# Performance work log

Measured on AMD Instinct MI355X. Metric: run time of the kernel, lower is better.

Reference implementation:

```python
import jax, jax.numpy as jnp
import numpy as np

N = 50000      # nodes
E = 800000     # edges (avg degree 16)
IN, H, OUT = 128, 128, 64
NEG_SLOPE = 0.01  # F.leaky_relu default


def _glorot(key, shape):
    lim = float(np.sqrt(6.0 / (shape[0] + shape[1])))
    return jax.random.uniform(key, shape, jnp.float32, -lim, lim)


def setup_inputs() -> dict:
    key = jax.random.key(0)
    ks = jax.random.split(key, 12)
    x = jax.random.normal(ks[0], (N, IN), jnp.float32)
    edge_index = jax.random.randint(ks[1], (2, E), 0, N, dtype=jnp.int64)
    edge_weight = jax.random.uniform(ks[2], (E,), jnp.float32)
    params = {}
    dims = [(IN, H), (H, H), (H, H), (H, OUT)]
    for i, (di, do) in enumerate(dims, start=1):
        params[f"W{i}"] = _glorot(ks[2 + i], (di, do))
        params[f"b{i}"] = jnp.zeros((do,), jnp.float32)
    return {"x": x, "edge_index": edge_index, "edge_weight": edge_weight, **params}


def _gcn_norm(edge_index, edge_weight, n):
    # PyG gcn_norm: add self-loops with weight 1, symmetric D^-1/2 A D^-1/2
    loop = jnp.arange(n, dtype=edge_index.dtype)
    row = jnp.concatenate([edge_index[0], loop])   # source
    col = jnp.concatenate([edge_index[1], loop])   # target
    w = jnp.concatenate([edge_weight, jnp.ones((n,), edge_weight.dtype)])
    deg = jax.ops.segment_sum(w, col, num_segments=n)
    dinv = jnp.where(deg > 0, jax.lax.rsqrt(deg), 0.0)
    norm = dinv[row] * w * dinv[col]
    return row, col, norm


def _gcn_conv(x, W, b, row, col, norm, n):
    h = x @ W                                   # [N, out] dense GEMM
    msg = h[row] * norm[:, None]                # gather + edge scale  [E+N, out]
    out = jax.ops.segment_sum(msg, col, num_segments=n)  # scatter-add
    return out + b


def reference(x, edge_index, edge_weight, W1, b1, W2, b2, W3, b3, W4, b4):
    n = x.shape[0]
    row, col, norm = _gcn_norm(edge_index, edge_weight, n)  # identical for all layers
    h = _gcn_conv(x, W1, b1, row, col, norm, n)
    h = jax.nn.leaky_relu(h, NEG_SLOPE)
    # dropout (p=0.25) is identity in eval mode
    h = _gcn_conv(h, W2, b2, row, col, norm, n)
    h = jax.nn.leaky_relu(h, NEG_SLOPE)
    h = _gcn_conv(h, W3, b3, row, col, norm, n)
    h = jax.nn.leaky_relu(h, NEG_SLOPE)
    h = _gcn_conv(h, W4, b4, row, col, norm, n)
    return h
```

## Files before the change

### kernel.cpp

```cpp
#include <hip/hip_runtime.h>
#include <hip/hip_bf16.h>


#define CAP 64


__global__ void fillcap_k(const int* __restrict__ ei, const float* __restrict__ ew,
                          int* __restrict__ fillc, int2* __restrict__ ed, int E) {
    int e = blockIdx.x * 256 + threadIdx.x;
    if (e >= E) return;
    int r = ei[e];
    int c = ei[E + e];
    int pos = atomicAdd(&fillc[c], 1);
    if (pos < CAP) {
        ed[(size_t)c * CAP + pos] = make_int2(r, __float_as_int(ew[e]));
    }
}

__global__ void segdeg_k(const int* __restrict__ fillc, const int2* __restrict__ ed,
                         float* __restrict__ dinv, int n) {
    int t = blockIdx.x * 256 + threadIdx.x;
    int node = t >> 4, l = t & 15;
    if (node >= n) return;
    int len = min(fillc[node], CAP);
    float s = 0.f;
    for (int i = l; i < len; i += 16) s += __int_as_float(ed[(size_t)node * CAP + i].y);
    #pragma unroll
    for (int d = 1; d < 16; d <<= 1) s += __shfl_xor(s, d);
    if (l == 0) dinv[node] = rsqrtf(s + 1.0f);
}

__global__ void nrmfix_k(const int* __restrict__ fillc, int2* __restrict__ ed,
                         const float* __restrict__ dinv, int n) {
    int t = blockIdx.x * 256 + threadIdx.x;
    int node = t >> 4, l = t & 15;
    if (node >= n) return;
    int len = min(fillc[node], CAP);
    float dc = dinv[node];
    for (int i = l; i < len; i += 16) {
        size_t idx = (size_t)node * CAP + i;
        int2 d = ed[idx];
        ((float*)&ed[idx])[1] = dinv[d.x] * __int_as_float(d.y) * dc;
    }
}


template <bool LEAKY>
__global__ __launch_bounds__(256) void aggcap128_k(
        const float* __restrict__ h, const int* __restrict__ fillc,
        const int2* __restrict__ ed, const float* __restrict__ dinv,
        const float* __restrict__ bias, float* __restrict__ out, int n) {
    int node = blockIdx.x * 4 + (threadIdx.x >> 6);
    if (node >= n) return;
    int lane = threadIdx.x & 63;
    int half = lane >> 5;
    int q = lane & 31;
    size_t beg = (size_t)node * CAP;
    int len = min(fillc[node], CAP);
    float4 acc = make_float4(0.f, 0.f, 0.f, 0.f);
    int e = 0;
    for (; e + 8 <= len; e += 8) {
        int2 d0 = ed[beg + e + 0 + half];
        int2 d1 = ed[beg + e + 2 + half];
        int2 d2 = ed[beg + e + 4 + half];
        int2 d3 = ed[beg + e + 6 + half];
        float4 v0 = *(const float4*)&h[(size_t)d0.x * 128 + q * 4];
        float4 v1 = *(const float4*)&h[(size_t)d1.x * 128 + q * 4];
        float4 v2 = *(const float4*)&h[(size_t)d2.x * 128 + q * 4];
        float4 v3 = *(const float4*)&h[(size_t)d3.x * 128 + q * 4];
        float w0 = __int_as_float(d0.y), w1 = __int_as_float(d1.y);
        float w2 = __int_as_float(d2.y), w3 = __int_as_float(d3.y);
        acc.x += w0*v0.x; acc.y += w0*v0.y; acc.z += w0*v0.z; acc.w += w0*v0.w;
        acc.x += w1*v1.x; acc.y += w1*v1.y; acc.z += w1*v1.z; acc.w += w1*v1.w;
        acc.x += w2*v2.x; acc.y += w2*v2.y; acc.z += w2*v2.z; acc.w += w2*v2.w;
        acc.x += w3*v3.x; acc.y += w3*v3.y; acc.z += w3*v3.z; acc.w += w3*v3.w;
    }
    if (e < len) {
        #pragma unroll
        for (int t = 0; t < 4; ++t) {
            int j = e + 2 * t + half;
            bool ok = j < len;
            int2 d = ed[beg + (ok ? j : 0)];
            float w = ok ? __int_as_float(d.y) : 0.f;
            int sr = ok ? d.x : node;
            float4 v = *(const float4*)&h[(size_t)sr * 128 + q * 4];
            acc.x += w*v.x; acc.y += w*v.y; acc.z += w*v.z; acc.w += w*v.w;
        }
    }
    acc.x += __shfl_xor(acc.x, 32);
    acc.y += __shfl_xor(acc.y, 32);
    acc.z += __shfl_xor(acc.z, 32);
    acc.w += __shfl_xor(acc.w, 32);
    float di = dinv[node];
    float ws = di * di;
    float4 hv = *(const float4*)&h[(size_t)node * 128 + q * 4];
    float4 bb = *(const float4*)&bias[q * 4];
    acc.x += ws*hv.x + bb.x;
    acc.y += ws*hv.y + bb.y;
    acc.z += ws*hv.z + bb.z;
    acc.w += ws*hv.w + bb.w;
    if (LEAKY) {
        acc.x = acc.x > 0.f ? acc.x : 0.01f * acc.x;
        acc.y = acc.y > 0.f ? acc.y : 0.01f * acc.y;
        acc.z = acc.z > 0.f ? acc.z : 0.01f * acc.z;
        acc.w = acc.w > 0.f ? acc.w : 0.01f * acc.w;
    }
    if (half == 0) *(float4*)&out[(size_t)node * 128 + q * 4] = acc;
}

__global__ __launch_bounds__(256) void aggcap64_k(
        const float* __restrict__ h, const int* __restrict__ fillc,
        const int2* __restrict__ ed, const float* __restrict__ dinv,
        const float* __restrict__ bias, float* __restrict__ out, int n) {
    int node = blockIdx.x * 4 + (threadIdx.x >> 6);
    if (node >= n) return;
    int lane = threadIdx.x & 63;
    int qtr = lane >> 4;
    int q = lane & 15;
    size_t beg = (size_t)node * CAP;
    int len = min(fillc[node], CAP);
    float4 acc = make_float4(0.f, 0.f, 0.f, 0.f);
    int e = 0;
    for (; e + 8 <= len; e += 8) {
        int2 d0 = ed[beg + e + 0 + qtr];
        int2 d1 = ed[beg + e + 4 + qtr];
        float4 v0 = *(const float4*)&h[(size_t)d0.x * 64 + q * 4];
        float4 v1 = *(const float4*)&h[(size_t)d1.x * 64 + q * 4];
        float w0 = __int_as_float(d0.y), w1 = __int_as_float(d1.y);
        acc.x += w0*v0.x; acc.y += w0*v0.y; acc.z += w0*v0.z; acc.w += w0*v0.w;
        acc.x += w1*v1.x; acc.y += w1*v1.y; acc.z += w1*v1.z; acc.w += w1*v1.w;
    }
    if (e < len) {
        #pragma unroll
        for (int t = 0; t < 2; ++t) {
            int j = e + 4 * t + qtr;
            bool ok = j < len;
            int2 d = ed[beg + (ok ? j : 0)];
            float w = ok ? __int_as_float(d.y) : 0.f;
            int sr = ok ? d.x : node;
            float4 v = *(const float4*)&h[(size_t)sr * 64 + q * 4];
            acc.x += w*v.x; acc.y += w*v.y; acc.z += w*v.z; acc.w += w*v.w;
        }
    }
    acc.x += __shfl_xor(acc.x, 16);
    acc.y += __shfl_xor(acc.y, 16);
    acc.z += __shfl_xor(acc.z, 16);
    acc.w += __shfl_xor(acc.w, 16);
    acc.x += __shfl_xor(acc.x, 32);
    acc.y += __shfl_xor(acc.y, 32);
    acc.z += __shfl_xor(acc.z, 32);
    acc.w += __shfl_xor(acc.w, 32);
    float di = dinv[node];
    float ws = di * di;
    float4 hv = *(const float4*)&h[(size_t)node * 64 + q * 4];
    float4 bb = *(const float4*)&bias[q * 4];
    acc.x += ws*hv.x + bb.x;
    acc.y += ws*hv.y + bb.y;
    acc.z += ws*hv.z + bb.z;
    acc.w += ws*hv.w + bb.w;
    if (qtr == 0) *(float4*)&out[(size_t)node * 64 + q * 4] = acc;
}


template <int OUTD>
__global__ __launch_bounds__(512) void gemm_k(const float* __restrict__ A,
                                              const float* __restrict__ W,
                                              float* __restrict__ C, int nrows) {
    constexpr int CW = OUTD / 16;
    constexpr int WF4 = (32 * OUTD / 4) / 512;
    __shared__ float As[32][132];
    __shared__ float Ws[32][OUTD];
    const int t = threadIdx.x;
    const int rowbase = blockIdx.x * 128;
    const int tx = t & 15, ty = t >> 4;
    const int r0 = ty * 4, c0 = tx * CW;

    float acc[4][CW];
    #pragma unroll
    for (int i = 0; i < 4; ++i)
        #pragma unroll
        for (int j = 0; j < CW; ++j) acc[i][j] = 0.f;

    const int arow0 = t >> 3, akq0 = t & 7;
    const int arow1 = (t + 512) >> 3, akq1 = t & 7;

    auto loadA = [&](int kt, int row, int kq) -> float4 {
        int gr = rowbase + row;
        if (gr < nrows) return *(const float4*)&A[(size_t)gr * 128 + kt * 32 + kq * 4];
        return make_float4(0.f, 0.f, 0.f, 0.f);
    };
    auto stA = [&](int row, int kq, float4 v) {
        As[kq * 4 + 0][row] = v.x;
        As[kq * 4 + 1][row] = v.y;
        As[kq * 4 + 2][row] = v.z;
        As[kq * 4 + 3][row] = v.w;
    };

    stA(arow0, akq0, loadA(0, arow0, akq0));
    stA(arow1, akq1, loadA(0, arow1, akq1));
    #pragma unroll
    for (int u = 0; u < WF4; ++u) {
        int idx = t + u * 512;
        int k = idx / (OUTD / 4), cq = idx % (OUTD / 4);
        *(float4*)&Ws[k][cq * 4] = *(const float4*)&W[(size_t)k * OUTD + cq * 4];
    }
    __syncthreads();

    float4 pa0, pa1, pw[WF4];
    #pragma unroll
    for (int kt = 0; kt < 4; ++kt) {
        if (kt < 3) {
            pa0 = loadA(kt + 1, arow0, akq0);
            pa1 = loadA(kt + 1, arow1, akq1);
            #pragma unroll
            for (int u = 0; u < WF4; ++u) {
                int idx = t + u * 512;
                int k = idx / (OUTD / 4), cq = idx % (OUTD / 4);
                pw[u] = *(const float4*)&W[(size_t)((kt + 1) * 32 + k) * OUTD + cq * 4];
            }
        }
        #pragma unroll 8
        for (int k = 0; k < 32; ++k) {
            float4 a = *(const float4*)&As[k][r0];
            float w[CW];
            #pragma unroll
            for (int j = 0; j < CW; j += 4)
                *(float4*)&w[j] = *(const float4*)&Ws[k][c0 + j];
            #pragma unroll
            for (int j = 0; j < CW; ++j) {
                acc[0][j] += a.x * w[j];
                acc[1][j] += a.y * w[j];
                acc[2][j] += a.z * w[j];
                acc[3][j] += a.w * w[j];
            }
        }
        __syncthreads();
        if (kt < 3) {
            stA(arow0, akq0, pa0);
            stA(arow1, akq1, pa1);
            #pragma unroll
            for (int u = 0; u < WF4; ++u) {
                int idx = t + u * 512;
                int k = idx / (OUTD / 4), cq = idx % (OUTD / 4);
                *(float4*)&Ws[k][cq * 4] = pw[u];
            }
            __syncthreads();
        }
    }

    #pragma unroll
    for (int i = 0; i < 4; ++i) {
        int gr = rowbase + r0 + i;
        if (gr < nrows) {
            #pragma unroll
            for (int j = 0; j < CW; j += 4)
                *(float4*)&C[(size_t)gr * OUTD + c0 + j] = *(float4*)&acc[i][j];
        }
    }
}


__global__ void deg_cnt_k(const int* __restrict__ ei, const float* __restrict__ ew,
                          float* __restrict__ deg, int* __restrict__ cnt, int E) {
    int e = blockIdx.x * 256 + threadIdx.x;
    if (e >= E) return;
    int c = ei[E + e];
    atomicAdd(&deg[c], ew[e]);
    atomicAdd(&cnt[c], 1);
}

__global__ void dinv_k(float* __restrict__ d, int n) {
    int i = blockIdx.x * 256 + threadIdx.x;
    if (i >= n) return;
    d[i] = rsqrtf(d[i] + 1.0f);
}

__global__ void scan_blocks_k(const int* __restrict__ cnt, int* __restrict__ rowptr,
                              int* __restrict__ partials, int n) {
    int gid = blockIdx.x * 1024 + threadIdx.x;
    int v = (gid < n) ? cnt[gid] : 0;
    int lane = threadIdx.x & 63, wid = threadIdx.x >> 6;
    int x = v;
    #pragma unroll
    for (int d = 1; d < 64; d <<= 1) {
        int y = __shfl_up(x, d);
        if (lane >= d) x += y;
    }
    __shared__ int wsum[16];
    if (lane == 63) wsum[wid] = x;
    __syncthreads();
    if (wid == 0 && lane < 16) {
        int s = wsum[lane];
        #pragma unroll
        for (int d = 1; d < 16; d <<= 1) {
            int y = __shfl_up(s, d);
            if (lane >= d) s += y;
        }
        wsum[lane] = s;
    }
    __syncthreads();
    int inc = x + (wid > 0 ? wsum[wid - 1] : 0);
    if (gid < n) rowptr[gid] = inc - v;
    if (threadIdx.x == 1023) partials[blockIdx.x] = inc;
}

__global__ void scan_part_k(int* __restrict__ p, int nb) {
    int lane = threadIdx.x;
    int v = (lane < nb) ? p[lane] : 0;
    int x = v;
    #pragma unroll
    for (int d = 1; d < 64; d <<= 1) {
        int y = __shfl_up(x, d);
        if (lane >= d) x += y;
    }
    if (lane < nb) p[lane] = x - v;
    if (lane == 63) p[nb] = x;
}

__global__ void scan_add_k(int* __restrict__ rowptr, const int* __restrict__ p,
                           int n, int nb) {
    int i = blockIdx.x * 1024 + threadIdx.x;
    if (i < n) rowptr[i] += p[blockIdx.x];
    if (i == 0) rowptr[n] = p[nb];
}

__global__ void fill_k(const int* __restrict__ ei, const float* __restrict__ ew,
                       const float* __restrict__ dinv, const int* __restrict__ rowptr,
                       int* __restrict__ fillc, int* __restrict__ src,
                       float* __restrict__ nrm, int E) {
    int e = blockIdx.x * 256 + threadIdx.x;
    if (e >= E) return;
    int r = ei[e];
    int c = ei[E + e];
    int pos = rowptr[c] + atomicAdd(&fillc[c], 1);
    src[pos] = r;
    nrm[pos] = dinv[r] * ew[e] * dinv[c];
}

template <bool LEAKY>
__global__ __launch_bounds__(256) void agg128_k(
        const float* __restrict__ h, const int* __restrict__ rowptr,
        const int* __restrict__ src, const float* __restrict__ nrm,
        const float* __restrict__ dinv, const float* __restrict__ bias,
        float* __restrict__ out, int n) {
    int node = blockIdx.x * 4 + (threadIdx.x >> 6);
    if (node >= n) return;
    int lane = threadIdx.x & 63;
    int beg = rowptr[node], end = rowptr[node + 1];
    float2 acc = make_float2(0.f, 0.f);
    int e = beg;
    for (; e + 4 <= end; e += 4) {
        int s0 = src[e], s1 = src[e + 1], s2 = src[e + 2], s3 = src[e + 3];
        float w0 = nrm[e], w1 = nrm[e + 1], w2 = nrm[e + 2], w3 = nrm[e + 3];
        float2 v0 = *(const float2*)&h[(size_t)s0 * 128 + lane * 2];
        float2 v1 = *(const float2*)&h[(size_t)s1 * 128 + lane * 2];
        float2 v2 = *(const float2*)&h[(size_t)s2 * 128 + lane * 2];
        float2 v3 = *(const float2*)&h[(size_t)s3 * 128 + lane * 2];
        acc.x += w0 * v0.x; acc.y += w0 * v0.y;
        acc.x += w1 * v1.x; acc.y += w1 * v1.y;
        acc.x += w2 * v2.x; acc.y += w2 * v2.y;
        acc.x += w3 * v3.x; acc.y += w3 * v3.y;
    }
    for (; e < end; ++e) {
        int s = src[e];
        float w = nrm[e];
        float2 hv = *(const float2*)&h[(size_t)s * 128 + lane * 2];
        acc.x += w * hv.x;
        acc.y += w * hv.y;
    }
    float di = dinv[node];
    float ws = di * di;
    float2 hv = *(const float2*)&h[(size_t)node * 128 + lane * 2];
    acc.x += ws * hv.x;
    acc.y += ws * hv.y;
    float2 bb = *(const float2*)&bias[lane * 2];
    acc.x += bb.x;
    acc.y += bb.y;
    if (LEAKY) {
        acc.x = acc.x > 0.f ? acc.x : 0.01f * acc.x;
        acc.y = acc.y > 0.f ? acc.y : 0.01f * acc.y;
    }
    *(float2*)&out[(size_t)node * 128 + lane * 2] = acc;
}

__global__ __launch_bounds__(256) void agg64_k(
        const float* __restrict__ h, const int* __restrict__ rowptr,
        const int* __restrict__ src, const float* __restrict__ nrm,
        const float* __restrict__ dinv, const float* __restrict__ bias,
        float* __restrict__ out, int n) {
    int node = blockIdx.x * 4 + (threadIdx.x >> 6);
    if (node >= n) return;
    int lane = threadIdx.x & 63;
    int beg = rowptr[node], end = rowptr[node + 1];
    float acc = 0.f;
    int e = beg;
    for (; e + 4 <= end; e += 4) {
        int s0 = src[e], s1 = src[e + 1], s2 = src[e + 2], s3 = src[e + 3];
        float w0 = nrm[e], w1 = nrm[e + 1], w2 = nrm[e + 2], w3 = nrm[e + 3];
        acc += w0 * h[(size_t)s0 * 64 + lane];
        acc += w1 * h[(size_t)s1 * 64 + lane];
        acc += w2 * h[(size_t)s2 * 64 + lane];
        acc += w3 * h[(size_t)s3 * 64 + lane];
    }
    for (; e < end; ++e) {
        acc += nrm[e] * h[(size_t)src[e] * 64 + lane];
    }
    float di = dinv[node];
    acc += di * di * h[(size_t)node * 64 + lane];
    acc += bias[lane];
    out[(size_t)node * 64 + lane] = acc;
}


extern "C" void kernel_launch(void* const* d_in, const int* in_sizes, int n_in,
                              void* d_out, int out_size, void* d_ws, size_t ws_size,
                              hipStream_t stream) {
    const float* x  = (const float*)d_in[0];
    const int* ei   = (const int*)d_in[1];
    const float* ew = (const float*)d_in[2];
    const float* W1 = (const float*)d_in[3];
    const float* b1 = (const float*)d_in[4];
    const float* W2 = (const float*)d_in[5];
    const float* b2 = (const float*)d_in[6];
    const float* W3 = (const float*)d_in[7];
    const float* b3 = (const float*)d_in[8];
    const float* W4 = (const float*)d_in[9];
    const float* b4 = (const float*)d_in[10];

    const int N = in_sizes[0] / 128;
    const int E = in_sizes[1] / 2;

    auto alignup = [](size_t o) { return (o + 255) & ~(size_t)255; };
    char* ws = (char*)d_ws;
    (void)n_in; (void)out_size;

    int eb = (E + 255) / 256;
    int gb = (N + 127) / 128;
    int ab = (N + 3) / 4;
    int qb = (N * 16 + 255) / 256;

    size_t off = 0;
    float* dinv  = (float*)(ws + off); off = alignup(off + (size_t)N * 4);
    int*   fillc = (int*)(ws + off);   off = alignup(off + (size_t)N * 4);
    size_t zb_cap = off;
    int2*  ed    = (int2*)(ws + off);  off = alignup(off + (size_t)N * CAP * 8);
    float* hbufC = (float*)(ws + off); off = alignup(off + (size_t)N * 128 * 4);
    float* featC = (float*)(ws + off); off = alignup(off + (size_t)N * 128 * 4);
    size_t need_cap = off;

    if (need_cap <= ws_size) {
        hipMemsetAsync(d_ws, 0, zb_cap, stream);
        fillcap_k<<<eb, 256, 0, stream>>>(ei, ew, fillc, ed, E);
        segdeg_k<<<qb, 256, 0, stream>>>(fillc, ed, dinv, N);
        nrmfix_k<<<qb, 256, 0, stream>>>(fillc, ed, dinv, N);

        gemm_k<128><<<gb, 512, 0, stream>>>(x, W1, hbufC, N);
        aggcap128_k<true><<<ab, 256, 0, stream>>>(hbufC, fillc, ed, dinv, b1, featC, N);
        gemm_k<128><<<gb, 512, 0, stream>>>(featC, W2, hbufC, N);
        aggcap128_k<true><<<ab, 256, 0, stream>>>(hbufC, fillc, ed, dinv, b2, featC, N);
        gemm_k<128><<<gb, 512, 0, stream>>>(featC, W3, hbufC, N);
        aggcap128_k<true><<<ab, 256, 0, stream>>>(hbufC, fillc, ed, dinv, b3, featC, N);
        gemm_k<64><<<gb, 512, 0, stream>>>(featC, W4, hbufC, N);
        aggcap64_k<<<ab, 256, 0, stream>>>(hbufC, fillc, ed, dinv, b4, (float*)d_out, N);
        return;
    }

    off = 0;
    float* deg   = (float*)(ws + off); off = alignup(off + (size_t)N * 4);
    int*   cnt   = (int*)(ws + off);   off = alignup(off + (size_t)N * 4);
    int*   fillc2= (int*)(ws + off);   off = alignup(off + (size_t)N * 4);
    size_t zbytes = off;
    int*   rowptr = (int*)(ws + off);  off = alignup(off + (size_t)(N + 1) * 4);
    int*   parts  = (int*)(ws + off);  off = alignup(off + 64 * 4);
    int*   srcA   = (int*)(ws + off);  off = alignup(off + (size_t)E * 4);
    float* nrm    = (float*)(ws + off); off = alignup(off + (size_t)E * 4);
    float* hbuf   = (float*)(ws + off); off = alignup(off + (size_t)N * 128 * 4);
    float* feat   = (float*)(ws + off); off = alignup(off + (size_t)N * 128 * 4);

    hipMemsetAsync(d_ws, 0, zbytes, stream);

    int nb = (N + 255) / 256;
    int sb = (N + 1023) / 1024;

    deg_cnt_k<<<eb, 256, 0, stream>>>(ei, ew, deg, cnt, E);
    dinv_k<<<nb, 256, 0, stream>>>(deg, N);
    scan_blocks_k<<<sb, 1024, 0, stream>>>(cnt, rowptr, parts, N);
    scan_part_k<<<1, 64, 0, stream>>>(parts, sb);
    scan_add_k<<<sb, 1024, 0, stream>>>(rowptr, parts, N, sb);
    fill_k<<<eb, 256, 0, stream>>>(ei, ew, deg, rowptr, fillc2, srcA, nrm, E);

    gemm_k<128><<<gb, 512, 0, stream>>>(x, W1, hbuf, N);
    agg128_k<true><<<ab, 256, 0, stream>>>(hbuf, rowptr, srcA, nrm, deg, b1, feat, N);
    gemm_k<128><<<gb, 512, 0, stream>>>(feat, W2, hbuf, N);
    agg128_k<true><<<ab, 256, 0, stream>>>(hbuf, rowptr, srcA, nrm, deg, b2, feat, N);
    gemm_k<128><<<gb, 512, 0, stream>>>(feat, W3, hbuf, N);
    agg128_k<true><<<ab, 256, 0, stream>>>(hbuf, rowptr, srcA, nrm, deg, b3, feat, N);
    gemm_k<64><<<gb, 512, 0, stream>>>(feat, W4, hbuf, N);
    agg64_k<<<ab, 256, 0, stream>>>(hbuf, rowptr, srcA, nrm, deg, b4, (float*)d_out, N);
}
```

Before: 377.9 us.

## Fuse first GEMM with edge bucketing, enlarge GEMM thread tiles, unroll aggregation

Merges the first-layer GEMM and the capped edge-bucket fill into one launch, with blocks split by blockIdx, so that independent work can overlap and one launch is removed. The GEMM moves from 512 to 256 threads per block, each thread now computing 8 rows instead of 4, with launch bounds targeting 3 blocks per CU. This gives more register reuse per shared-memory load at the cost of higher register pressure. The aggregation kernels gain a 16-edge unrolled loop that issues more independent gathers per iteration to hide memory latency.

```diff
diff --git a/kernel.cpp b/kernel.cpp
--- a/kernel.cpp
+++ b/kernel.cpp
@@ -4,6 +4,128 @@
 
 #define CAP 64
 
+
+template <int OUTD>
+__device__ __forceinline__ void gemm_body(const float* __restrict__ A,
+                                          const float* __restrict__ W,
+                                          float* __restrict__ C, int nrows, int bid) {
+    constexpr int CW = OUTD / 16;
+    constexpr int WF4 = (32 * OUTD / 4) / 256;
+    __shared__ float As[32][132];
+    __shared__ float Ws[32][OUTD];
+    const int t = threadIdx.x;
+    const int rowbase = bid * 128;
+    const int tx = t & 15, ty = t >> 4;
+    const int r0 = ty * 8, c0 = tx * CW;
+
+    float acc[8][CW];
+    #pragma unroll
+    for (int i = 0; i < 8; ++i)
+        #pragma unroll
+        for (int j = 0; j < CW; ++j) acc[i][j] = 0.f;
+
+    const int arow = t >> 3, akq = t & 7;
+
+    auto loadA = [&](int kt, int row) -> float4 {
+        int gr = rowbase + row;
+        if (gr < nrows) return *(const float4*)&A[(size_t)gr * 128 + kt * 32 + akq * 4];
+        return make_float4(0.f, 0.f, 0.f, 0.f);
+    };
+    auto stA = [&](int row, float4 v) {
+        As[akq * 4 + 0][row] = v.x;
+        As[akq * 4 + 1][row] = v.y;
+        As[akq * 4 + 2][row] = v.z;
+        As[akq * 4 + 3][row] = v.w;
+    };
+
+    #pragma unroll
+    for (int u = 0; u < 4; ++u) stA(arow + u * 32, loadA(0, arow + u * 32));
+    #pragma unroll
+    for (int u = 0; u < WF4; ++u) {
+        int idx = t + u * 256;
+        int k = idx / (OUTD / 4), cq = idx % (OUTD / 4);
+        *(float4*)&Ws[k][cq * 4] = *(const float4*)&W[(size_t)k * OUTD + cq * 4];
+    }
+    __syncthreads();
+
+    float4 pa[4], pw[WF4];
+    #pragma unroll
+    for (int kt = 0; kt < 4; ++kt) {
+        if (kt < 3) {
+            #pragma unroll
+            for (int u = 0; u < 4; ++u) pa[u] = loadA(kt + 1, arow + u * 32);
+            #pragma unroll
+            for (int u = 0; u < WF4; ++u) {
+                int idx = t + u * 256;
+                int k = idx / (OUTD / 4), cq = idx % (OUTD / 4);
+                pw[u] = *(const float4*)&W[(size_t)((kt + 1) * 32 + k) * OUTD + cq * 4];
+            }
+        }
+        #pragma unroll 8
+        for (int k = 0; k < 32; ++k) {
+            float4 a0 = *(const float4*)&As[k][r0];
+            float4 a1 = *(const float4*)&As[k][r0 + 4];
+            float w[CW];
+            #pragma unroll
+            for (int j = 0; j < CW; j += 4)
+                *(float4*)&w[j] = *(const float4*)&Ws[k][c0 + j];
+            float ar[8] = {a0.x, a0.y, a0.z, a0.w, a1.x, a1.y, a1.z, a1.w};
+            #pragma unroll
+            for (int i = 0; i < 8; ++i)
+                #pragma unroll
+                for (int j = 0; j < CW; ++j)
+                    acc[i][j] += ar[i] * w[j];
+        }
+        __syncthreads();
+        if (kt < 3) {
+            #pragma unroll
+            for (int u = 0; u < 4; ++u) stA(arow + u * 32, pa[u]);
+            #pragma unroll
+            for (int u = 0; u < WF4; ++u) {
+                int idx = t + u * 256;
+                int k = idx / (OUTD / 4), cq = idx % (OUTD / 4);
+                *(float4*)&Ws[k][cq * 4] = pw[u];
+            }
+            __syncthreads();
+        }
+    }
+
+    #pragma unroll
+    for (int i = 0; i < 8; ++i) {
+        int gr = rowbase + r0 + i;
+        if (gr < nrows) {
+            #pragma unroll
+            for (int j = 0; j < CW; j += 4)
+                *(float4*)&C[(size_t)gr * OUTD + c0 + j] = *(float4*)&acc[i][j];
+        }
+    }
+}
+
+template <int OUTD>
+__global__ __launch_bounds__(256, 3) void gemm_k(const float* __restrict__ A,
+                                                 const float* __restrict__ W,
+                                                 float* __restrict__ C, int nrows) {
+    gemm_body<OUTD>(A, W, C, nrows, blockIdx.x);
+}
+
+__global__ __launch_bounds__(256, 3) void gemm1_fill_k(
+        const float* __restrict__ A, const float* __restrict__ W,
+        float* __restrict__ C, int nrows, int gb,
+        const int* __restrict__ ei, const float* __restrict__ ew,
+        int* __restrict__ fillc, int2* __restrict__ ed, int E) {
+    if ((int)blockIdx.x < gb) {
+        gemm_body<128>(A, W, C, nrows, blockIdx.x);
+        return;
+    }
+    int e = (blockIdx.x - gb) * 256 + threadIdx.x;
+    if (e >= E) return;
+    int r = ei[e];
+    int c = ei[E + e];
+    int pos = atomicAdd(&fillc[c], 1);
+    if (pos < CAP) {
+        ed[(size_t)c * CAP + pos] = make_int2(r, __float_as_int(ew[e]));
+    }
+}
 
 __global__ void fillcap_k(const int* __restrict__ ei, const float* __restrict__ ew,
                           int* __restrict__ fillc, int2* __restrict__ ed, int E) {
@@ -59,6 +181,21 @@
     int len = min(fillc[node], CAP);
     float4 acc = make_float4(0.f, 0.f, 0.f, 0.f);
     int e = 0;
+    for (; e + 16 <= len; e += 16) {
+        int2 d[8];
+        #pragma unroll
+        for (int u = 0; u < 8; ++u) d[u] = ed[beg + e + 2 * u + half];
+        float4 v[8];
+        #pragma unroll
+        for (int u = 0; u < 8; ++u)
+            v[u] = *(const float4*)&h[(size_t)d[u].x * 128 + q * 4];
+        #pragma unroll
+        for (int u = 0; u < 8; ++u) {
+            float w = __int_as_float(d[u].y);
+            acc.x += w * v[u].x; acc.y += w * v[u].y;
+            acc.z += w * v[u].z; acc.w += w * v[u].w;
+        }
+    }
     for (; e + 8 <= len; e += 8) {
         int2 d0 = ed[beg + e + 0 + half];
         int2 d1 = ed[beg + e + 2 + half];
@@ -121,6 +258,21 @@
     int len = min(fillc[node], CAP);
     float4 acc = make_float4(0.f, 0.f, 0.f, 0.f);
     int e = 0;
+    for (; e + 16 <= len; e += 16) {
+        int2 d[4];
+        #pragma unroll
+        for (int u = 0; u < 4; ++u) d[u] = ed[beg + e + 4 * u + qtr];
+        float4 v[4];
+        #pragma unroll
+        for (int u = 0; u < 4; ++u)
+            v[u] = *(const float4*)&h[(size_t)d[u].x * 64 + q * 4];
+        #pragma unroll
+        for (int u = 0; u < 4; ++u) {
+            float w = __int_as_float(d[u].y);
+            acc.x += w * v[u].x; acc.y += w * v[u].y;
+            acc.z += w * v[u].z; acc.w += w * v[u].w;
+        }
+    }
     for (; e + 8 <= len; e += 8) {
         int2 d0 = ed[beg + e + 0 + qtr];
         int2 d1 = ed[beg + e + 4 + qtr];
@@ -159,104 +311,6 @@
     acc.z += ws*hv.z + bb.z;
     acc.w += ws*hv.w + bb.w;
     if (qtr == 0) *(float4*)&out[(size_t)node * 64 + q * 4] = acc;
-}
-
-
-template <int OUTD>
-__global__ __launch_bounds__(512) void gemm_k(const float* __restrict__ A,
-                                              const float* __restrict__ W,
-                                              float* __restrict__ C, int nrows) {
-    constexpr int CW = OUTD / 16;
-    constexpr int WF4 = (32 * OUTD / 4) / 512;
-    __shared__ float As[32][132];
-    __shared__ float Ws[32][OUTD];
-    const int t = threadIdx.x;
-    const int rowbase = blockIdx.x * 128;
-    const int tx = t & 15, ty = t >> 4;
-    const int r0 = ty * 4, c0 = tx * CW;
-
-    float acc[4][CW];
-    #pragma unroll
-    for (int i = 0; i < 4; ++i)
-        #pragma unroll
-        for (int j = 0; j < CW; ++j) acc[i][j] = 0.f;
-
-    const int arow0 = t >> 3, akq0 = t & 7;
-    const int arow1 = (t + 512) >> 3, akq1 = t & 7;
-
-    auto loadA = [&](int kt, int row, int kq) -> float4 {
-        int gr = rowbase + row;
-        if (gr < nrows) return *(const float4*)&A[(size_t)gr * 128 + kt * 32 + kq * 4];
-        return make_float4(0.f, 0.f, 0.f, 0.f);
-    };
-    auto stA = [&](int row, int kq, float4 v) {
-        As[kq * 4 + 0][row] = v.x;
-        As[kq * 4 + 1][row] = v.y;
-        As[kq * 4 + 2][row] = v.z;
-        As[kq * 4 + 3][row] = v.w;
-    };
-
-    stA(arow0, akq0, loadA(0, arow0, akq0));
-    stA(arow1, akq1, loadA(0, arow1, akq1));
-    #pragma unroll
-    for (int u = 0; u < WF4; ++u) {
-        int idx = t + u * 512;
-        int k = idx / (OUTD / 4), cq = idx % (OUTD / 4);
-        *(float4*)&Ws[k][cq * 4] = *(const float4*)&W[(size_t)k * OUTD + cq * 4];
-    }
-    __syncthreads();
-
-    float4 pa0, pa1, pw[WF4];
-    #pragma unroll
-    for (int kt = 0; kt < 4; ++kt) {
-        if (kt < 3) {
-            pa0 = loadA(kt + 1, arow0, akq0);
-            pa1 = loadA(kt + 1, arow1, akq1);
-            #pragma unroll
-            for (int u = 0; u < WF4; ++u) {
-                int idx = t + u * 512;
-                int k = idx / (OUTD / 4), cq = idx % (OUTD / 4);
-                pw[u] = *(const float4*)&W[(size_t)((kt + 1) * 32 + k) * OUTD + cq * 4];
-            }
-        }
-        #pragma unroll 8
-        for (int k = 0; k < 32; ++k) {
-            float4 a = *(const float4*)&As[k][r0];
-            float w[CW];
-            #pragma unroll
-            for (int j = 0; j < CW; j += 4)
-                *(float4*)&w[j] = *(const float4*)&Ws[k][c0 + j];
-            #pragma unroll
-            for (int j = 0; j < CW; ++j) {
-                acc[0][j] += a.x * w[j];
-                acc[1][j] += a.y * w[j];
-                acc[2][j] += a.z * w[j];
-                acc[3][j] += a.w * w[j];
-            }
-        }
-        __syncthreads();
-        if (kt < 3) {
-            stA(arow0, akq0, pa0);
-            stA(arow1, akq1, pa1);
-            #pragma unroll
-            for (int u = 0; u < WF4; ++u) {
-                int idx = t + u * 512;
-                int k = idx / (OUTD / 4), cq = idx % (OUTD / 4);
-                *(float4*)&Ws[k][cq * 4] = pw[u];
-            }
-            __syncthreads();
-        }
-    }
-
-    #pragma unroll
-    for (int i = 0; i < 4; ++i) {
-        int gr = rowbase + r0 + i;
-        if (gr < nrows) {
-            #pragma unroll
-            for (int j = 0; j < CW; j += 4)
-                *(float4*)&C[(size_t)gr * OUTD + c0 + j] = *(float4*)&acc[i][j];
-        }
-    }
 }
 
 
@@ -450,17 +504,17 @@
 
     if (need_cap <= ws_size) {
         hipMemsetAsync(d_ws, 0, zb_cap, stream);
-        fillcap_k<<<eb, 256, 0, stream>>>(ei, ew, fillc, ed, E);
+        gemm1_fill_k<<<gb + eb, 256, 0, stream>>>(x, W1, hbufC, N, gb,
+                                                  ei, ew, fillc, ed, E);
         segdeg_k<<<qb, 256, 0, stream>>>(fillc, ed, dinv, N);
         nrmfix_k<<<qb, 256, 0, stream>>>(fillc, ed, dinv, N);
 
-        gemm_k<128><<<gb, 512, 0, stream>>>(x, W1, hbufC, N);
         aggcap128_k<true><<<ab, 256, 0, stream>>>(hbufC, fillc, ed, dinv, b1, featC, N);
-        gemm_k<128><<<gb, 512, 0, stream>>>(featC, W2, hbufC, N);
+        gemm_k<128><<<gb, 256, 0, stream>>>(featC, W2, hbufC, N);
         aggcap128_k<true><<<ab, 256, 0, stream>>>(hbufC, fillc, ed, dinv, b2, featC, N);
-        gemm_k<128><<<gb, 512, 0, stream>>>(featC, W3, hbufC, N);
+        gemm_k<128><<<gb, 256, 0, stream>>>(featC, W3, hbufC, N);
         aggcap128_k<true><<<ab, 256, 0, stream>>>(hbufC, fillc, ed, dinv, b3, featC, N);
-        gemm_k<64><<<gb, 512, 0, stream>>>(featC, W4, hbufC, N);
+        gemm_k<64><<<gb, 256, 0, stream>>>(featC, W4, hbufC, N);
         aggcap64_k<<<ab, 256, 0, stream>>>(hbufC, fillc, ed, dinv, b4, (float*)d_out, N);
         return;
     }
@@ -489,12 +543,12 @@
     scan_add_k<<<sb, 1024, 0, stream>>>(rowptr, parts, N, sb);
     fill_k<<<eb, 256, 0, stream>>>(ei, ew, deg, rowptr, fillc2, srcA, nrm, E);
 
-    gemm_k<128><<<gb, 512, 0, stream>>>(x, W1, hbuf, N);
+    gemm_k<128><<<gb, 256, 0, stream>>>(x, W1, hbuf, N);
     agg128_k<true><<<ab, 256, 0, stream>>>(hbuf, rowptr, srcA, nrm, deg, b1, feat, N);
-    gemm_k<128><<<gb, 512, 0, stream>>>(feat, W2, hbuf, N);
+    gemm_k<128><<<gb, 256, 0, stream>>>(feat, W2, hbuf, N);
     agg128_k<true><<<ab, 256, 0, stream>>>(hbuf, rowptr, srcA, nrm, deg, b2, feat, N);
-    gemm_k<128><<<gb, 512, 0, stream>>>(feat, W3, hbuf, N);
+    gemm_k<128><<<gb, 256, 0, stream>>>(feat, W3, hbuf, N);
     agg128_k<true><<<ab, 256, 0, stream>>>(hbuf, rowptr, srcA, nrm, deg, b3, feat, N);
-    gemm_k<64><<<gb, 512, 0, stream>>>(feat, W4, hbuf, N);
+    gemm_k<64><<<gb, 256, 0, stream>>>(feat, W4, hbuf, N);
     agg64_k<<<ab, 256, 0, stream>>>(hbuf, rowptr, srcA, nrm, deg, b4, (float*)d_out, N);
 }
```

Result: faster. 360.7 us (-4.5%).
